# Performance work log

Measured on AMD Instinct MI355X. Metric: run time of the kernel, lower is better.

Reference implementation:

```python
import jax, jax.numpy as jnp
import numpy as np

S, N, DIN, DH, C, K, E = 12, 50000, 64, 128, 2, 3, 600000
HID = (DH + C) // 2  # 65
LN_EPS = 1e-5


def setup_inputs() -> dict:
    key = jax.random.key(0)
    ks = jax.random.split(key, 16)
    sc = 0.05
    inp = {
        'H': jax.random.normal(ks[0], (S, N, DIN), dtype=jnp.float32),
        'edge_index': jax.random.randint(ks[1], (2, E), 0, N, dtype=jnp.int64),
        # stacked gate params, gate order: 0=i, 1=f, 2=c(cell), 3=o
        'Wx': jax.random.normal(ks[2], (4, K, DIN, DH), dtype=jnp.float32) * sc,
        'bx': jnp.zeros((4, DH), dtype=jnp.float32),
        'Wh': jax.random.normal(ks[3], (4, K, DH, DH), dtype=jnp.float32) * sc,
        'bh': jnp.zeros((4, DH), dtype=jnp.float32),
        'b_gate': jnp.zeros((4, DH), dtype=jnp.float32),
        'wc': jax.random.normal(ks[4], (3, DH), dtype=jnp.float32) * sc,  # peephole: i, f, o
        'ln_gamma': jnp.ones((DH,), dtype=jnp.float32),
        'ln_beta': jnp.zeros((DH,), dtype=jnp.float32),
        'W1': jax.random.normal(ks[5], (DH, HID), dtype=jnp.float32) * sc,
        'b1': jnp.zeros((HID,), dtype=jnp.float32),
        'W2': jax.random.normal(ks[6], (HID, C), dtype=jnp.float32) * sc,
        'b2': jnp.zeros((C,), dtype=jnp.float32),
    }
    return inp


def _cheb_norm(edge_index):
    # sym-normalized, lambda_max=2 => scaled Laplacian Lhat = -D^-1/2 A D^-1/2 (zero diagonal)
    src, dst = edge_index[0], edge_index[1]
    ones = jnp.ones((src.shape[0],), dtype=jnp.float32)
    deg = jax.ops.segment_sum(ones, src, num_segments=N)
    dinv = jnp.where(deg > 0, jax.lax.rsqrt(jnp.maximum(deg, 1.0)), 0.0)
    norm = -dinv[src] * dinv[dst]
    return src, dst, norm


def _cheb_conv(x, W, b, src, dst, norm):
    # x: [N, Din]; W: [K, Din, Dout]. T0=x, T1=Lhat x, Tk=2 Lhat T_{k-1} - T_{k-2}
    Tx0 = x
    out = Tx0 @ W[0]
    if K > 1:
        Tx1 = jax.ops.segment_sum(norm[:, None] * Tx0[src], dst, num_segments=N)
        out = out + Tx1 @ W[1]
        for k in range(2, K):
            Tx2 = 2.0 * jax.ops.segment_sum(norm[:, None] * Tx1[src], dst, num_segments=N) - Tx0
            out = out + Tx2 @ W[k]
            Tx0, Tx1 = Tx1, Tx2
    return out + b


def _decoder(H, edge_index, Wx, bx, Wh, bh, b_gate, wc, ln_gamma, ln_beta, W1, b1, W2, b2):
    src, dst, norm = _cheb_norm(edge_index)

    def step(carry, x_t):
        h, c = carry
        gx = lambda g: _cheb_conv(x_t, Wx[g], bx[g], src, dst, norm)
        gh = lambda g: _cheb_conv(h, Wh[g], bh[g], src, dst, norm)
        i = jax.nn.sigmoid(gx(0) + gh(0) + wc[0] * c + b_gate[0])
        f = jax.nn.sigmoid(gx(1) + gh(1) + wc[1] * c + b_gate[1])
        t = jnp.tanh(gx(2) + gh(2) + b_gate[2])
        c = f * c + i * t
        o = jax.nn.sigmoid(gx(3) + gh(3) + wc[2] * c + b_gate[3])
        h = o * jnp.tanh(c)
        return (h, c), h

    h0 = jnp.zeros((N, DH), dtype=H.dtype)
    (_, _), X = jax.lax.scan(step, (h0, h0), H)  # X: [S, N, DH]

    X = jnp.tanh(X)
    # LayerNorm over conv_dim (last axis here)
    mu = jnp.mean(X, axis=-1, keepdims=True)
    var = jnp.mean(jnp.square(X - mu), axis=-1, keepdims=True)
    X = (X - mu) * jax.lax.rsqrt(var + LN_EPS) * ln_gamma + ln_beta
    # dropout in eval mode: identity
    X = jax.nn.relu(X @ W1 + b1) @ W2 + b2  # [S, N, C]
    X = jax.nn.sigmoid(X)
    return jnp.transpose(X, (1, 2, 0))  # [N, C, S]


def reference(H, edge_index, Wx, bx, Wh, bh, b_gate, wc, ln_gamma, ln_beta, W1, b1, W2, b2):
    return _decoder(H, edge_index, Wx, bx, Wh, bh, b_gate, wc, ln_gamma, ln_beta, W1, b1, W2, b2)
```

## Files before the change

### kernel.cpp

```cpp
#include <hip/hip_runtime.h>
#include <cstdint>
#include <cstddef>

#define S_DIM 12
#define N_NODE 50000
#define N_PAD 50048
#define N_P2 50176
#define D_IN 64
#define D_H 128
#define N_E 600000
#define K_TOT 576
#define N_COL 512
#define HID_P 80
#define N_HID 65
#define AXC 192

typedef short bf16x8 __attribute__((ext_vector_type(8)));
typedef float f32x4 __attribute__((ext_vector_type(4)));

__device__ __forceinline__ float bf2f(unsigned short u){
  union { unsigned int i; float f; } v; v.i = ((unsigned int)u) << 16; return v.f;
}
__device__ __forceinline__ unsigned short f2bf(float f){
  union { float f; unsigned int i; } v; v.f = f;
  unsigned int x = v.i;
  return (unsigned short)((x + 0x7fffu + ((x >> 16) & 1u)) >> 16);
}
__device__ __forceinline__ float sigf(float x){ return 1.f/(1.f + __expf(-x)); }
__device__ __forceinline__ float ftanh(float x){
  x = fminf(fmaxf(x, -12.f), 12.f);
  float e = __expf(2.f*x);
  return (e - 1.f)/(e + 1.f);
}

__device__ __forceinline__ void gload16(const void* g, void* lds){
  __builtin_amdgcn_global_load_lds((const __attribute__((address_space(1))) unsigned int*)g,
                                   (__attribute__((address_space(3))) unsigned int*)lds, 16, 0, 0);
}

__device__ __forceinline__ void acc12(float* a, uint2 p0, uint2 p1, uint2 p2, float w){
  unsigned int u[6] = {p0.x, p0.y, p1.x, p1.y, p2.x, p2.y};
#pragma unroll
  for (int i=0;i<6;++i){
    a[2*i]   += w * bf2f((unsigned short)(u[i] & 0xffffu));
    a[2*i+1] += w * bf2f((unsigned short)(u[i] >> 16));
  }
}
__device__ __forceinline__ void acc8(float* a, uint4 h, float w){
  unsigned int u[4] = {h.x, h.y, h.z, h.w};
#pragma unroll
  for (int i=0;i<4;++i){
    a[2*i]   += w * bf2f((unsigned short)(u[i] & 0xffffu));
    a[2*i+1] += w * bf2f((unsigned short)(u[i] >> 16));
  }
}

__global__ void k_prep(const float* __restrict__ Wx, const float* __restrict__ Wh,
                       const float* __restrict__ bx, const float* __restrict__ bh,
                       const float* __restrict__ bg, const float* __restrict__ W1,
                       const float* __restrict__ b1, const float* __restrict__ W2,
                       unsigned short* __restrict__ Bct, float* __restrict__ btot,
                       unsigned short* __restrict__ W1t, float* __restrict__ b1p,
                       float* __restrict__ W2p)
{
  int idx = blockIdx.x*256 + threadIdx.x;
  if (idx < N_COL*K_TOT){
    int cc = idx / K_TOT, k = idx - cc*K_TOT;
    int g = (cc>>4)&3, d = (cc&15) + ((cc>>6)<<4);
    float v;
    if (k < 384){
      int kt = k >> 7, j = k & 127;
      const float* Wg = Wh + (size_t)g*3*128*128;
      if (kt == 0)      v = Wg[(size_t)j*128 + d] - Wg[(size_t)(256+j)*128 + d];
      else if (kt == 1) v = Wg[(size_t)(128+j)*128 + d];
      else              v = 2.f*Wg[(size_t)(256+j)*128 + d];
    } else {
      int kk = k - 384; int kt = kk >> 6, j = kk & 63;
      const float* Wg = Wx + (size_t)g*3*64*128;
      if (kt == 0)      v = Wg[(size_t)j*128 + d] - Wg[(size_t)(128+j)*128 + d];
      else if (kt == 1) v = Wg[(size_t)(64+j)*128 + d];
      else              v = 2.f*Wg[(size_t)(128+j)*128 + d];
    }
    Bct[(size_t)cc*K_TOT + k] = f2bf(v);
  }
  if (idx < N_COL) btot[idx] = bx[idx] + bh[idx] + bg[idx];
  if (idx < HID_P*D_H){ int c = idx >> 7, k = idx & 127;
    W1t[idx] = (c < N_HID) ? f2bf(W1[k*N_HID + c]) : (unsigned short)0; }
  if (idx < HID_P) b1p[idx] = (idx < N_HID) ? b1[idx] : 0.f;
  if (idx < HID_P*2){ int c = idx >> 1, j = idx & 1; W2p[idx] = (c < N_HID) ? W2[c*2 + j] : 0.f; }
}

__global__ void k_xprep(const float* __restrict__ H, unsigned short* __restrict__ Xtr,
                        unsigned short* __restrict__ Axt){
  int idx = blockIdx.x*256 + threadIdx.x;
  if (idx >= N_PAD*64) return;
  int n = idx >> 6, d = idx & 63;
  union { unsigned short u[12]; uint2 q[3]; } pk;
  if (n < N_NODE){
#pragma unroll
    for (int t=0;t<12;++t) pk.u[t] = f2bf(H[((size_t)t*N_NODE + n)*64 + d]);
  } else {
#pragma unroll
    for (int t=0;t<12;++t) pk.u[t] = 0;
  }
  uint2* xp = (uint2*)(Xtr + (size_t)idx*12);
  xp[0]=pk.q[0]; xp[1]=pk.q[1]; xp[2]=pk.q[2];
#pragma unroll
  for (int t=0;t<12;++t) Axt[((size_t)t*N_PAD + n)*AXC + d] = pk.u[t];
  if (n >= N_NODE){
#pragma unroll
    for (int t=0;t<12;++t){
      Axt[((size_t)t*N_PAD + n)*AXC + 64 + d]  = 0;
      Axt[((size_t)t*N_PAD + n)*AXC + 128 + d] = 0;
    }
  }
}

__global__ void k_deg(const int* __restrict__ ei, int* __restrict__ dsrc, int* __restrict__ ddst){
  int e = blockIdx.x*256 + threadIdx.x;
  if (e < N_E){
    atomicAdd(&dsrc[ei[e]], 1);
    atomicAdd(&ddst[ei[N_E + e]], 1);
  }
}
__global__ void k_dinv(const int* __restrict__ dsrc, float* __restrict__ dinv){
  int n = blockIdx.x*256 + threadIdx.x;
  if (n < N_P2) dinv[n] = (dsrc[n] > 0) ? rsqrtf((float)dsrc[n]) : 0.f;
}
__global__ void k_scan1(const int* __restrict__ in, int* __restrict__ outp, int* __restrict__ part){
  __shared__ int sm[256];
  int tid = threadIdx.x;
  int i = blockIdx.x*256 + tid;
  int v = in[i];
  int x = v;
  sm[tid] = x; __syncthreads();
  for (int off=1; off<256; off<<=1){
    int y = (tid >= off) ? sm[tid-off] : 0;
    __syncthreads();
    x += y; sm[tid] = x; __syncthreads();
  }
  outp[i] = x - v;
  if (tid == 255) part[blockIdx.x] = x;
}
__global__ void k_scan2(int* __restrict__ part, int nblk){
  __shared__ int sm[256];
  int tid = threadIdx.x;
  int v = (tid < nblk) ? part[tid] : 0;
// ... 9 lines not shown
  int i = blockIdx.x*256 + threadIdx.x;
  offs[i] = outp[i] + part[blockIdx.x];
}
__global__ void k_csr(const int* __restrict__ ei, const float* __restrict__ dinv,
                      const int* __restrict__ offs, int* __restrict__ cursor,
                      int2* __restrict__ cedge){
  int e = blockIdx.x*256 + threadIdx.x;
  if (e < N_E){
    int s = ei[e], d = ei[N_E + e];
    int pos = atomicAdd(&cursor[d], 1);
    float w = -dinv[s]*dinv[d];
    cedge[offs[d] + pos] = make_int2(s, __float_as_int(w));
  }
}

__global__ void k_xspmm1(const unsigned short* __restrict__ Xtr, unsigned short* __restrict__ Axt,
                         unsigned short* __restrict__ U1tr,
                         const int* __restrict__ offs, const int2* __restrict__ cedge){
  int n = blockIdx.x*4 + (threadIdx.x >> 6);
  int l = threadIdx.x & 63;
  if (n >= N_NODE) return;
  int beg = offs[n], end = offs[n+1];
  int ce = end - 1;
  float a[12];
#pragma unroll
  for (int t=0;t<12;++t) a[t] = 0.f;
  for (int q = beg; q < end; q += 6){
    int2 e0 = cedge[min(q,   ce)];
    int2 e1 = cedge[min(q+1, ce)];
    int2 e2 = cedge[min(q+2, ce)];
    int2 e3 = cedge[min(q+3, ce)];
    int2 e4 = cedge[min(q+4, ce)];
    int2 e5 = cedge[min(q+5, ce)];
    float w0 = __int_as_float(e0.y);
    float w1 = (q+1 < end) ? __int_as_float(e1.y) : 0.f;
    float w2 = (q+2 < end) ? __int_as_float(e2.y) : 0.f;
    float w3 = (q+3 < end) ? __int_as_float(e3.y) : 0.f;
    float w4 = (q+4 < end) ? __int_as_float(e4.y) : 0.f;
    float w5 = (q+5 < end) ? __int_as_float(e5.y) : 0.f;
    const uint2* r0 = (const uint2*)(Xtr + ((size_t)e0.x*64 + l)*12);
    const uint2* r1 = (const uint2*)(Xtr + ((size_t)e1.x*64 + l)*12);
    const uint2* r2 = (const uint2*)(Xtr + ((size_t)e2.x*64 + l)*12);
    const uint2* r3 = (const uint2*)(Xtr + ((size_t)e3.x*64 + l)*12);
    const uint2* r4 = (const uint2*)(Xtr + ((size_t)e4.x*64 + l)*12);
    const uint2* r5 = (const uint2*)(Xtr + ((size_t)e5.x*64 + l)*12);
    uint2 p00=r0[0], p01=r0[1], p02=r0[2];
    uint2 p10=r1[0], p11=r1[1], p12=r1[2];
    uint2 p20=r2[0], p21=r2[1], p22=r2[2];
    uint2 p30=r3[0], p31=r3[1], p32=r3[2];
    uint2 p40=r4[0], p41=r4[1], p42=r4[2];
    uint2 p50=r5[0], p51=r5[1], p52=r5[2];
    acc12(a, p00, p01, p02, w0);
    acc12(a, p10, p11, p12, w1);
    acc12(a, p20, p21, p22, w2);
    acc12(a, p30, p31, p32, w3);
    acc12(a, p40, p41, p42, w4);
    acc12(a, p50, p51, p52, w5);
  }
  union { unsigned short u[12]; uint2 qq[3]; } pk;
#pragma unroll
  for (int t=0;t<12;++t){
    unsigned short b = f2bf(a[t]);
    pk.u[t] = b;
    Axt[((size_t)t*N_PAD + n)*AXC + 64 + l] = b;
  }
  uint2* op = (uint2*)(U1tr + ((size_t)n*64 + l)*12);
  op[0]=pk.qq[0]; op[1]=pk.qq[1]; op[2]=pk.qq[2];
}
__global__ void k_xspmm2(const unsigned short* __restrict__ U1tr, unsigned short* __restrict__ Axt,
                         const int* __restrict__ offs, const int2* __restrict__ cedge){
  int n = blockIdx.x*4 + (threadIdx.x >> 6);
  int l = threadIdx.x & 63;
  if (n >= N_NODE) return;
  int beg = offs[n], end = offs[n+1];
  int ce = end - 1;
  float a[12];
#pragma unroll
  for (int t=0;t<12;++t) a[t] = 0.f;
  for (int q = beg; q < end; q += 6){
    int2 e0 = cedge[min(q,   ce)];
    int2 e1 = cedge[min(q+1, ce)];
    int2 e2 = cedge[min(q+2, ce)];
    int2 e3 = cedge[min(q+3, ce)];
    int2 e4 = cedge[min(q+4, ce)];
    int2 e5 = cedge[min(q+5, ce)];
    float w0 = __int_as_float(e0.y);
    float w1 = (q+1 < end) ? __int_as_float(e1.y) : 0.f;
    float w2 = (q+2 < end) ? __int_as_float(e2.y) : 0.f;
    float w3 = (q+3 < end) ? __int_as_float(e3.y) : 0.f;
    float w4 = (q+4 < end) ? __int_as_float(e4.y) : 0.f;
    float w5 = (q+5 < end) ? __int_as_float(e5.y) : 0.f;
    const uint2* r0 = (const uint2*)(U1tr + ((size_t)e0.x*64 + l)*12);
    const uint2* r1 = (const uint2*)(U1tr + ((size_t)e1.x*64 + l)*12);
    const uint2* r2 = (const uint2*)(U1tr + ((size_t)e2.x*64 + l)*12);
    const uint2* r3 = (const uint2*)(U1tr + ((size_t)e3.x*64 + l)*12);
    const uint2* r4 = (const uint2*)(U1tr + ((size_t)e4.x*64 + l)*12);
    const uint2* r5 = (const uint2*)(U1tr + ((size_t)e5.x*64 + l)*12);
    uint2 p00=r0[0], p01=r0[1], p02=r0[2];
    uint2 p10=r1[0], p11=r1[1], p12=r1[2];
    uint2 p20=r2[0], p21=r2[1], p22=r2[2];
    uint2 p30=r3[0], p31=r3[1], p32=r3[2];
    uint2 p40=r4[0], p41=r4[1], p42=r4[2];
    uint2 p50=r5[0], p51=r5[1], p52=r5[2];
    acc12(a, p00, p01, p02, w0);
    acc12(a, p10, p11, p12, w1);
    acc12(a, p20, p21, p22, w2);
    acc12(a, p30, p31, p32, w3);
    acc12(a, p40, p41, p42, w4);
    acc12(a, p50, p51, p52, w5);
  }
#pragma unroll
  for (int t=0;t<12;++t)
    Axt[((size_t)t*N_PAD + n)*AXC + 128 + l] = f2bf(a[t]);
}

__global__ void k_spmm1(const unsigned short* __restrict__ Hc, unsigned short* __restrict__ U,
                        const int* __restrict__ offs, const int2* __restrict__ cedge){
  int n = blockIdx.x*4 + (threadIdx.x >> 6);
  int l = threadIdx.x & 63;
  if (n >= N_NODE) return;
  int sub = l >> 4, fl = l & 15;
  int beg = offs[n], end = offs[n+1];
  int ce = end - 1;
  float a[8];
#pragma unroll
  for (int j=0;j<8;++j) a[j] = 0.f;
  for (int q = beg; q < end; q += 16){
    int i0 = q + sub, i1 = q + 4 + sub, i2 = q + 8 + sub, i3 = q + 12 + sub;
    int2 e0 = cedge[min(i0, ce)];
    int2 e1 = cedge[min(i1, ce)];
    int2 e2 = cedge[min(i2, ce)];
    int2 e3 = cedge[min(i3, ce)];
    float w0 = (i0 < end) ? __int_as_float(e0.y) : 0.f;
    float w1 = (i1 < end) ? __int_as_float(e1.y) : 0.f;
// ... 8 lines not shown
    acc8(a, h2, w2);
    acc8(a, h3, w3);
  }
#pragma unroll
  for (int j=0;j<8;++j){
    a[j] += __shfl_xor(a[j], 16);
    a[j] += __shfl_xor(a[j], 32);
  }
  if (sub == 0){
    unsigned short o[8];
#pragma unroll
    for (int j=0;j<8;++j) o[j] = f2bf(a[j]);
    *(uint4*)(U + (size_t)n*256 + fl*8) = *(const uint4*)o;
  }
}
__global__ void k_spmm2(unsigned short* __restrict__ U,
                        const int* __restrict__ offs, const int2* __restrict__ cedge){
  int n = blockIdx.x*4 + (threadIdx.x >> 6);
  int l = threadIdx.x & 63;
  if (n >= N_NODE) return;
  int sub = l >> 4, fl = l & 15;
  int beg = offs[n], end = offs[n+1];
  int ce = end - 1;
  float a[8];
#pragma unroll
  for (int j=0;j<8;++j) a[j] = 0.f;
  for (int q = beg; q < end; q += 16){
    int i0 = q + sub, i1 = q + 4 + sub, i2 = q + 8 + sub, i3 = q + 12 + sub;
    int2 e0 = cedge[min(i0, ce)];
    int2 e1 = cedge[min(i1, ce)];
// ... 13 lines not shown
    acc8(a, h3, w3);
  }
#pragma unroll
  for (int j=0;j<8;++j){
    a[j] += __shfl_xor(a[j], 16);
    a[j] += __shfl_xor(a[j], 32);
  }
  if (sub == 0){
    unsigned short o[8];
#pragma unroll
    for (int j=0;j<8;++j) o[j] = f2bf(a[j]);
    *(uint4*)(U + (size_t)n*256 + 128 + fl*8) = *(const uint4*)o;
  }
}

__global__ __launch_bounds__(256,2) void k_gemm(
    const unsigned short* __restrict__ Hc, const unsigned short* __restrict__ U,
    const unsigned short* __restrict__ Axt,
    const unsigned short* __restrict__ Bct, const float* __restrict__ btot,
    const float* __restrict__ wc, float* __restrict__ c, unsigned short* __restrict__ Hn)
{
  __shared__ __align__(16) unsigned short As[2][128*64];
  __shared__ __align__(16) unsigned short Bs[2][128*64];
  int tid = threadIdx.x;
  int w = tid >> 6, l = tid & 63;
  const int NWG = 1564, q8 = NWG >> 3, r8 = NWG & 7;
  int L = blockIdx.y*4 + blockIdx.x;
  int xcd = L & 7, li = L >> 3;
  int W = (xcd < r8 ? xcd*(q8+1) : r8*(q8+1) + (xcd-r8)*q8) + li;
  int bx = W & 3, by = W >> 2;
  int n0 = bx * 128;
  int m0 = by * 128;
  const f32x4 vzero = {0.f,0.f,0.f,0.f};
  f32x4 acc[4][4];
#pragma unroll
  for (int i=0;i<4;++i)
#pragma unroll
    for (int j=0;j<4;++j) acc[i][j] = vzero;
  int wr = w >> 1, wn = w & 1;

  auto stage = [&](int buf, int it){
    const unsigned short* Ab; int astr, acol;
    if (it < 2)      { Ab = Hc;  astr = 128; acol = it*64; }
    else if (it < 6) { Ab = U;   astr = 256; acol = (it-2)*64; }
    else             { Ab = Axt; astr = AXC; acol = (it-6)*64; }
#pragma unroll
    for (int i=0;i<4;++i){
      int rr = w*32 + i*8;
      int row = rr + (l>>3);
      gload16(Ab  + (size_t)(m0+row)*astr + acol + (l&7)*8, (void*)(As[buf] + rr*64));
      gload16(Bct + (size_t)(n0+row)*K_TOT + it*64 + (l&7)*8, (void*)(Bs[buf] + rr*64));
    }
  };

  stage(0, 0);
  __syncthreads();
  for (int it=0; it<9; ++it){
    int cur = it & 1;
    if (it < 8) stage(cur^1, it+1);
#pragma unroll
    for (int kk=0; kk<2; ++kk){
      bf16x8 af[4], bfv[4];
#pragma unroll
      for (int i=0;i<4;++i) af[i]  = *(const bf16x8*)(As[cur] + (wr*64 + i*16 + (l&15))*64 + kk*32 + (l>>4)*8);
#pragma unroll
      for (int j=0;j<4;++j) bfv[j] = *(const bf16x8*)(Bs[cur] + (wn*64 + j*16 + (l&15))*64 + kk*32 + (l>>4)*8);
#pragma unroll
      for (int i=0;i<4;++i)
#pragma unroll
        for (int j=0;j<4;++j)
          acc[i][j] = __builtin_amdgcn_mfma_f32_16x16x32_bf16(af[i], bfv[j], acc[i][j], 0,0,0);
    }
    __syncthreads();
  }
  int dd = (((bx<<1) + wn) << 4) | (l & 15);
  float b_i = btot[dd], b_f = btot[128+dd], b_t = btot[256+dd], b_o = btot[384+dd];
  float wci = wc[dd], wcf = wc[128+dd], wco = wc[256+dd];
#pragma unroll
  for (int i=0;i<4;++i){
    int row0 = m0 + wr*64 + i*16 + (l>>4)*4;
#pragma unroll
    for (int r=0;r<4;++r){
      int row = row0 + r;
      float co = c[(size_t)row*128 + dd];
      float gi = sigf(acc[i][0][r] + b_i + wci*co);
      float gf = sigf(acc[i][1][r] + b_f + wcf*co);
      float tt = ftanh(acc[i][2][r] + b_t);
      float cn = gf*co + gi*tt;
      float go = sigf(acc[i][3][r] + b_o + wco*cn);
      float h = go * ftanh(cn);
      c[(size_t)row*128 + dd] = cn;
      Hn[(size_t)row*128 + dd] = f2bf(h);
    }
  }
}

__global__ __launch_bounds__(256,2) void k_lnmlp(const unsigned short* __restrict__ Hn,
                        const unsigned short* __restrict__ W1t, const float* __restrict__ b1p,
                        const float* __restrict__ W2p, const float* __restrict__ b2,
                        const float* __restrict__ gam, const float* __restrict__ bet,
                        float* __restrict__ out, int t)
{
  __shared__ __align__(16) unsigned short xn[64*128];
  __shared__ __align__(16) unsigned short w1s[HID_P*128];
  __shared__ float w2s[HID_P*2];
  __shared__ float b1s[HID_P];
  __shared__ float b2s[2];
  int tid = threadIdx.x;
  for (int i = tid; i < HID_P*128/8; i += 256) ((int4*)w1s)[i] = ((const int4*)W1t)[i];
  if (tid < HID_P*2) w2s[tid] = W2p[tid];
  if (tid < HID_P)   b1s[tid] = b1p[tid];
  if (tid < 2)       b2s[tid] = b2[tid];
  int n0 = blockIdx.x*64;
  int row = tid >> 2, part = tid & 3;
  int n = n0 + row;
  float vals[32];
  float s = 0.f, ss = 0.f;
  if (n < N_NODE){
    const unsigned short* hp = Hn + (size_t)n*128 + part*32;
#pragma unroll
    for (int k=0;k<32;++k){
      float x = ftanh(bf2f(hp[k]));
      vals[k] = x; s += x; ss += x*x;
    }
  } else {
#pragma unroll
    for (int k=0;k<32;++k) vals[k] = 0.f;
  }
  s  += __shfl_xor(s,1);  s  += __shfl_xor(s,2);
  ss += __shfl_xor(ss,1); ss += __shfl_xor(ss,2);
  float mu = s * (1.f/128.f);
  float var = ss * (1.f/128.f) - mu*mu;
  float inv = rsqrtf(fmaxf(var, 0.f) + 1e-5f);
#pragma unroll
  for (int k=0;k<32;++k){
    int d = part*32 + k;
    xn[row*128 + d] = f2bf((vals[k]-mu)*inv*gam[d] + bet[d]);
  }
  __syncthreads();
  int w = tid >> 6, l = tid & 63;
  const f32x4 vzero = {0.f,0.f,0.f,0.f};
  f32x4 acc[5];
#pragma unroll
  for (int tj=0;tj<5;++tj) acc[tj] = vzero;
#pragma unroll
  for (int kk=0;kk<4;++kk){
    bf16x8 a = *(const bf16x8*)(xn + (w*16 + (l&15))*128 + kk*32 + (l>>4)*8);
#pragma unroll
    for (int tj=0;tj<5;++tj){
      bf16x8 b = *(const bf16x8*)(w1s + (tj*16 + (l&15))*128 + kk*32 + (l>>4)*8);
      acc[tj] = __builtin_amdgcn_mfma_f32_16x16x32_bf16(a, b, acc[tj], 0,0,0);
    }
  }
#pragma unroll
  for (int r=0;r<4;++r){
    int rn = n0 + w*16 + (l>>4)*4 + r;
    float p0 = 0.f, p1 = 0.f;
#pragma unroll
    for (int tj=0;tj<5;++tj){
      int col = tj*16 + (l&15);
      float hv = fmaxf(acc[tj][r] + b1s[col], 0.f);
      p0 += hv * w2s[col*2];
      p1 += hv * w2s[col*2+1];
    }
    p0 += __shfl_xor(p0,1); p0 += __shfl_xor(p0,2); p0 += __shfl_xor(p0,4); p0 += __shfl_xor(p0,8);
    p1 += __shfl_xor(p1,1); p1 += __shfl_xor(p1,2); p1 += __shfl_xor(p1,4); p1 += __shfl_xor(p1,8);
    if ((l & 15) == 0 && rn < N_NODE){
      float* op = out + (size_t)rn*24 + t;
      op[0]  = sigf(p0 + b2s[0]);
      op[12] = sigf(p1 + b2s[1]);
    }
  }
}

extern "C" void kernel_launch(void* const* d_in, const int* in_sizes, int n_in,
                              void* d_out, int out_size, void* d_ws, size_t ws_size,
                              hipStream_t stream)
{
  const float* H   = (const float*)d_in[0];
  const int*   ei  = (const int*)d_in[1];
  const float* Wx  = (const float*)d_in[2];
  const float* bx  = (const float*)d_in[3];
  const float* Wh  = (const float*)d_in[4];
  const float* bh  = (const float*)d_in[5];
  const float* bg  = (const float*)d_in[6];
  const float* wc  = (const float*)d_in[7];
  const float* gam = (const float*)d_in[8];
  const float* bet = (const float*)d_in[9];
  const float* W1  = (const float*)d_in[10];
  const float* b1  = (const float*)d_in[11];
  const float* W2  = (const float*)d_in[12];
  const float* b2  = (const float*)d_in[13];
  float* out = (float*)d_out;
  (void)in_sizes; (void)n_in; (void)out_size; (void)ws_size;

  char* p = (char*)d_ws;
  auto alloc = [&](size_t bytes)->char*{ char* r = p; p += (bytes + 255) & ~(size_t)255; return r; };
  char* zbase = p;
  float*          c_st  = (float*)alloc((size_t)N_PAD*128*4);
  unsigned short* Hbuf0 = (unsigned short*)alloc((size_t)N_PAD*128*2);
  unsigned short* Ubuf  = (unsigned short*)alloc((size_t)N_PAD*256*2);
  int* dsrc   = (int*)alloc((size_t)N_P2*4);
  int* ddst   = (int*)alloc((size_t)N_P2*4);
  int* cursor = (int*)alloc((size_t)N_P2*4);
  size_t zbytes = (size_t)(p - zbase);
  unsigned short* Hbuf1 = (unsigned short*)alloc((size_t)N_PAD*128*2);
  unsigned short* Xtr   = (unsigned short*)alloc((size_t)N_PAD*64*12*2);
  unsigned short* U1tr  = (unsigned short*)alloc((size_t)N_PAD*64*12*2);
  unsigned short* Axt   = (unsigned short*)alloc((size_t)S_DIM*N_PAD*AXC*2);
  unsigned short* Bct   = (unsigned short*)alloc((size_t)N_COL*K_TOT*2);
  float*          btot  = (float*)alloc(N_COL*4);
  unsigned short* W1t   = (unsigned short*)alloc(HID_P*128*2);
  float*          b1p   = (float*)alloc(HID_P*4);
  float*          W2p   = (float*)alloc(HID_P*2*4);
  float*          dinv  = (float*)alloc((size_t)N_P2*4);
  int*            offs  = (int*)alloc((size_t)(N_P2+256)*4);
  int*            outp  = (int*)alloc((size_t)N_P2*4);
  int*            partb = (int*)alloc(256*4);
  int2*           cedge = (int2*)alloc((size_t)N_E*8);

  hipMemsetAsync(zbase, 0, zbytes, stream);
  k_prep<<<(N_COL*K_TOT + 255)/256, 256, 0, stream>>>(Wx, Wh, bx, bh, bg, W1, b1, W2,
                                                      Bct, btot, W1t, b1p, W2p);
  k_xprep<<<(N_PAD*64 + 255)/256, 256, 0, stream>>>(H, Xtr, Axt);
  k_deg<<<(N_E + 255)/256, 256, 0, stream>>>(ei, dsrc, ddst);
  k_dinv<<<N_P2/256, 256, 0, stream>>>(dsrc, dinv);
  k_scan1<<<N_P2/256, 256, 0, stream>>>(ddst, outp, partb);
  k_scan2<<<1, 256, 0, stream>>>(partb, N_P2/256);
  k_scan3<<<N_P2/256, 256, 0, stream>>>(outp, partb, offs);
  k_csr<<<(N_E + 255)/256, 256, 0, stream>>>(ei, dinv, offs, cursor, cedge);
  k_xspmm1<<<N_NODE/4, 256, 0, stream>>>(Xtr, Axt, U1tr, offs, cedge);
  k_xspmm2<<<N_NODE/4, 256, 0, stream>>>(U1tr, Axt, offs, cedge);

  for (int t = 0; t < S_DIM; ++t){
    unsigned short* Hc = (t & 1) ? Hbuf1 : Hbuf0;
    unsigned short* Hn = (t & 1) ? Hbuf0 : Hbuf1;
    if (t > 0){
      k_spmm1<<<N_NODE/4, 256, 0, stream>>>(Hc, Ubuf, offs, cedge);
      k_spmm2<<<N_NODE/4, 256, 0, stream>>>(Ubuf, offs, cedge);
    }
    k_gemm<<<dim3(4, N_PAD/128), 256, 0, stream>>>(Hc, Ubuf,
        Axt + (size_t)t*N_PAD*AXC, Bct, btot, wc, c_st, Hn);
    k_lnmlp<<<N_PAD/64, 256, 0, stream>>>(Hn, W1t, b1p, W2p, b2, gam, bet, out, t);
  }
}
```

Before: 1.976 ms.

## Merge setup kernels, fuse spmm1 with LN-MLP, split x-SpMM halves, single-buffer GEMM

Folds the weight prep, input transpose and degree counting into one multi-role launch, and folds the dinv computation into the first scan pass. The first SpMM of each timestep now runs in the same launch as the LayerNorm+MLP of the previous step. The x-path SpMMs are split into two 6-timestep halves to cut register use. The GEMM drops its LDS double buffering and skips the zero hidden-state part at step 0. The aim is fewer launches and more overlap of independent work. The cost is that loads are no longer overlapped with MFMA inside the GEMM.

Result: faster. 1.860 ms (-5.9%).

```diff
diff --git a/kernel.cpp b/kernel.cpp
--- a/kernel.cpp
+++ b/kernel.cpp
@@ -15,6 +15,12 @@
 #define N_HID 65
 #define AXC 192
 
+#define NB_PREP 1152
+#define NB_XPREP 12512
+#define NB_DEG 2344
+#define NB_SPMM 12500
+#define NB_LN 782
+
 typedef short bf16x8 __attribute__((ext_vector_type(8)));
 typedef float f32x4 __attribute__((ext_vector_type(4)));
 
@@ -32,16 +38,14 @@
   float e = __expf(2.f*x);
   return (e - 1.f)/(e + 1.f);
 }
-
 __device__ __forceinline__ void gload16(const void* g, void* lds){
   __builtin_amdgcn_global_load_lds((const __attribute__((address_space(1))) unsigned int*)g,
                                    (__attribute__((address_space(3))) unsigned int*)lds, 16, 0, 0);
 }
-
-__device__ __forceinline__ void acc12(float* a, uint2 p0, uint2 p1, uint2 p2, float w){
-  unsigned int u[6] = {p0.x, p0.y, p1.x, p1.y, p2.x, p2.y};
-#pragma unroll
-  for (int i=0;i<6;++i){
+__device__ __forceinline__ void acc6(float* a, unsigned int p0, unsigned int p1, unsigned int p2, float w){
+  unsigned int u[3] = {p0, p1, p2};
+#pragma unroll
+  for (int i=0;i<3;++i){
     a[2*i]   += w * bf2f((unsigned short)(u[i] & 0xffffu));
     a[2*i+1] += w * bf2f((unsigned short)(u[i] >> 16));
   }
@@ -55,82 +59,86 @@
   }
 }
 
-__global__ void k_prep(const float* __restrict__ Wx, const float* __restrict__ Wh,
-                       const float* __restrict__ bx, const float* __restrict__ bh,
-                       const float* __restrict__ bg, const float* __restrict__ W1,
-                       const float* __restrict__ b1, const float* __restrict__ W2,
-                       unsigned short* __restrict__ Bct, float* __restrict__ btot,
-                       unsigned short* __restrict__ W1t, float* __restrict__ b1p,
-                       float* __restrict__ W2p)
+__global__ void k_setup(const float* __restrict__ H, const int* __restrict__ ei,
+                        const float* __restrict__ Wx, const float* __restrict__ Wh,
+                        const float* __restrict__ bx, const float* __restrict__ bh,
+                        const float* __restrict__ bg, const float* __restrict__ W1,
+                        const float* __restrict__ b1, const float* __restrict__ W2,
+                        unsigned short* __restrict__ Bct, float* __restrict__ btot,
+                        unsigned short* __restrict__ W1t, float* __restrict__ b1p,
+                        float* __restrict__ W2p, unsigned short* __restrict__ Xtr,
+                        unsigned short* __restrict__ Axt,
+                        int* __restrict__ dsrc, int* __restrict__ ddst)
 {
-  int idx = blockIdx.x*256 + threadIdx.x;
-  if (idx < N_COL*K_TOT){
-    int cc = idx / K_TOT, k = idx - cc*K_TOT;
-    int g = (cc>>4)&3, d = (cc&15) + ((cc>>6)<<4);
-    float v;
-    if (k < 384){
-      int kt = k >> 7, j = k & 127;
-      const float* Wg = Wh + (size_t)g*3*128*128;
-      if (kt == 0)      v = Wg[(size_t)j*128 + d] - Wg[(size_t)(256+j)*128 + d];
-      else if (kt == 1) v = Wg[(size_t)(128+j)*128 + d];
-      else              v = 2.f*Wg[(size_t)(256+j)*128 + d];
+  int bb = blockIdx.x, tid = threadIdx.x;
+  if (bb < NB_PREP){
+    int idx = bb*256 + tid;
+    if (idx < N_COL*K_TOT){
+      int cc = idx / K_TOT, k = idx - cc*K_TOT;
+      int g = (cc>>4)&3, d = (cc&15) + ((cc>>6)<<4);
+      float v;
+      if (k < 384){
+        int kt = k >> 7, j = k & 127;
+        const float* Wg = Wh + (size_t)g*3*128*128;
+        if (kt == 0)      v = Wg[(size_t)j*128 + d] - Wg[(size_t)(256+j)*128 + d];
+        else if (kt == 1) v = Wg[(size_t)(128+j)*128 + d];
+        else              v = 2.f*Wg[(size_t)(256+j)*128 + d];
+      } else {
+        int kk = k - 384; int kt = kk >> 6, j = kk & 63;
+        const float* Wg = Wx + (size_t)g*3*64*128;
+        if (kt == 0)      v = Wg[(size_t)j*128 + d] - Wg[(size_t)(128+j)*128 + d];
+        else if (kt == 1) v = Wg[(size_t)(64+j)*128 + d];
+        else              v = 2.f*Wg[(size_t)(128+j)*128 + d];
+      }
+      Bct[(size_t)cc*K_TOT + k] = f2bf(v);
+    }
+    if (idx < N_COL) btot[idx] = bx[idx] + bh[idx] + bg[idx];
+    if (idx < HID_P*D_H){ int c = idx >> 7, k = idx & 127;
+      W1t[idx] = (c < N_HID) ? f2bf(W1[k*N_HID + c]) : (unsigned short)0; }
+    if (idx < HID_P) b1p[idx] = (idx < N_HID) ? b1[idx] : 0.f;
+    if (idx < HID_P*2){ int c = idx >> 1, j = idx & 1; W2p[idx] = (c < N_HID) ? W2[c*2 + j] : 0.f; }
+  } else if (bb < NB_PREP + NB_XPREP){
+    int idx = (bb - NB_PREP)*256 + tid;
+    int n = idx >> 6, d = idx & 63;
+    unsigned short u[12];
+    if (n < N_NODE){
+#pragma unroll
+      for (int t=0;t<12;++t) u[t] = f2bf(H[((size_t)t*N_NODE + n)*64 + d]);
     } else {
-      int kk = k - 384; int kt = kk >> 6, j = kk & 63;
-      const float* Wg = Wx + (size_t)g*3*64*128;
-      if (kt == 0)      v = Wg[(size_t)j*128 + d] - Wg[(size_t)(128+j)*128 + d];
-      else if (kt == 1) v = Wg[(size_t)(64+j)*128 + d];
-      else              v = 2.f*Wg[(size_t)(128+j)*128 + d];
-    }
-    Bct[(size_t)cc*K_TOT + k] = f2bf(v);
-  }
-  if (idx < N_COL) btot[idx] = bx[idx] + bh[idx] + bg[idx];
-  if (idx < HID_P*D_H){ int c = idx >> 7, k = idx & 127;
-    W1t[idx] = (c < N_HID) ? f2bf(W1[k*N_HID + c]) : (unsigned short)0; }
-  if (idx < HID_P) b1p[idx] = (idx < N_HID) ? b1[idx] : 0.f;
-  if (idx < HID_P*2){ int c = idx >> 1, j = idx & 1; W2p[idx] = (c < N_HID) ? W2[c*2 + j] : 0.f; }
-}
-
-__global__ void k_xprep(const float* __restrict__ H, unsigned short* __restrict__ Xtr,
-                        unsigned short* __restrict__ Axt){
-  int idx = blockIdx.x*256 + threadIdx.x;
-  if (idx >= N_PAD*64) return;
-  int n = idx >> 6, d = idx & 63;
-  union { unsigned short u[12]; uint2 q[3]; } pk;
-  if (n < N_NODE){
-#pragma unroll
-    for (int t=0;t<12;++t) pk.u[t] = f2bf(H[((size_t)t*N_NODE + n)*64 + d]);
+#pragma unroll
+      for (int t=0;t<12;++t) u[t] = 0;
+    }
+    unsigned int* x0 = (unsigned int*)(Xtr + (size_t)idx*6);
+    unsigned int* x1 = (unsigned int*)(Xtr + (size_t)N_PAD*384 + (size_t)idx*6);
+#pragma unroll
+    for (int i=0;i<3;++i){
+      x0[i] = (unsigned int)u[2*i]   | ((unsigned int)u[2*i+1] << 16);
+      x1[i] = (unsigned int)u[6+2*i] | ((unsigned int)u[6+2*i+1] << 16);
+    }
+#pragma unroll
+    for (int t=0;t<12;++t) Axt[((size_t)t*N_PAD + n)*AXC + d] = u[t];
+    if (n >= N_NODE){
+#pragma unroll
+      for (int t=0;t<12;++t){
+        Axt[((size_t)t*N_PAD + n)*AXC + 64 + d]  = 0;
+        Axt[((size_t)t*N_PAD + n)*AXC + 128 + d] = 0;
+      }
+    }
   } else {
-#pragma unroll
-    for (int t=0;t<12;++t) pk.u[t] = 0;
-  }
-  uint2* xp = (uint2*)(Xtr + (size_t)idx*12);
-  xp[0]=pk.q[0]; xp[1]=pk.q[1]; xp[2]=pk.q[2];
-#pragma unroll
-  for (int t=0;t<12;++t) Axt[((size_t)t*N_PAD + n)*AXC + d] = pk.u[t];
-  if (n >= N_NODE){
-#pragma unroll
-    for (int t=0;t<12;++t){
-      Axt[((size_t)t*N_PAD + n)*AXC + 64 + d]  = 0;
-      Axt[((size_t)t*N_PAD + n)*AXC + 128 + d] = 0;
-    }
-  }
-}
-
-__global__ void k_deg(const int* __restrict__ ei, int* __restrict__ dsrc, int* __restrict__ ddst){
-  int e = blockIdx.x*256 + threadIdx.x;
-  if (e < N_E){
-    atomicAdd(&dsrc[ei[e]], 1);
-    atomicAdd(&ddst[ei[N_E + e]], 1);
-  }
-}
-__global__ void k_dinv(const int* __restrict__ dsrc, float* __restrict__ dinv){
-  int n = blockIdx.x*256 + threadIdx.x;
-  if (n < N_P2) dinv[n] = (dsrc[n] > 0) ? rsqrtf((float)dsrc[n]) : 0.f;
-}
-__global__ void k_scan1(const int* __restrict__ in, int* __restrict__ outp, int* __restrict__ part){
+    int e = (bb - NB_PREP - NB_XPREP)*256 + tid;
+    if (e < N_E){
+      atomicAdd(&dsrc[ei[e]], 1);
+      atomicAdd(&ddst[ei[N_E + e]], 1);
+    }
+  }
+}
+
+__global__ void k_scan1d(const int* __restrict__ in, int* __restrict__ outp, int* __restrict__ part,
+                         const int* __restrict__ dsrc, float* __restrict__ dinv){
   __shared__ int sm[256];
   int tid = threadIdx.x;
   int i = blockIdx.x*256 + tid;
+  dinv[i] = (dsrc[i] > 0) ? rsqrtf((float)dsrc[i]) : 0.f;
   int v = in[i];
   int x = v;
   sm[tid] = x; __syncthreads();
@@ -170,17 +178,17 @@
   }
 }
 
-__global__ void k_xspmm1(const unsigned short* __restrict__ Xtr, unsigned short* __restrict__ Axt,
-                         unsigned short* __restrict__ U1tr,
+__global__ void k_xspmm1(const unsigned short* __restrict__ Xh, unsigned short* __restrict__ AxtH,
+                         unsigned short* __restrict__ Uh,
                          const int* __restrict__ offs, const int2* __restrict__ cedge){
   int n = blockIdx.x*4 + (threadIdx.x >> 6);
   int l = threadIdx.x & 63;
   if (n >= N_NODE) return;
   int beg = offs[n], end = offs[n+1];
   int ce = end - 1;
-  float a[12];
-#pragma unroll
-  for (int t=0;t<12;++t) a[t] = 0.f;
+  float a[6];
+#pragma unroll
+  for (int t=0;t<6;++t) a[t] = 0.f;
   for (int q = beg; q < end; q += 6){
     int2 e0 = cedge[min(q,   ce)];
     int2 e1 = cedge[min(q+1, ce)];
@@ -194,45 +202,45 @@
     float w3 = (q+3 < end) ? __int_as_float(e3.y) : 0.f;
     float w4 = (q+4 < end) ? __int_as_float(e4.y) : 0.f;
     float w5 = (q+5 < end) ? __int_as_float(e5.y) : 0.f;
-    const uint2* r0 = (const uint2*)(Xtr + ((size_t)e0.x*64 + l)*12);
-    const uint2* r1 = (const uint2*)(Xtr + ((size_t)e1.x*64 + l)*12);
-    const uint2* r2 = (const uint2*)(Xtr + ((size_t)e2.x*64 + l)*12);
-    const uint2* r3 = (const uint2*)(Xtr + ((size_t)e3.x*64 + l)*12);
-    const uint2* r4 = (const uint2*)(Xtr + ((size_t)e4.x*64 + l)*12);
-    const uint2* r5 = (const uint2*)(Xtr + ((size_t)e5.x*64 + l)*12);
-    uint2 p00=r0[0], p01=r0[1], p02=r0[2];
-    uint2 p10=r1[0], p11=r1[1], p12=r1[2];
-    uint2 p20=r2[0], p21=r2[1], p22=r2[2];
-    uint2 p30=r3[0], p31=r3[1], p32=r3[2];
-    uint2 p40=r4[0], p41=r4[1], p42=r4[2];
-    uint2 p50=r5[0], p51=r5[1], p52=r5[2];
-    acc12(a, p00, p01, p02, w0);
-    acc12(a, p10, p11, p12, w1);
-    acc12(a, p20, p21, p22, w2);
-    acc12(a, p30, p31, p32, w3);
-    acc12(a, p40, p41, p42, w4);
-    acc12(a, p50, p51, p52, w5);
-  }
-  union { unsigned short u[12]; uint2 qq[3]; } pk;
-#pragma unroll
-  for (int t=0;t<12;++t){
-    unsigned short b = f2bf(a[t]);
-    pk.u[t] = b;
-    Axt[((size_t)t*N_PAD + n)*AXC + 64 + l] = b;
-  }
-  uint2* op = (uint2*)(U1tr + ((size_t)n*64 + l)*12);
-  op[0]=pk.qq[0]; op[1]=pk.qq[1]; op[2]=pk.qq[2];
-}
-__global__ void k_xspmm2(const unsigned short* __restrict__ U1tr, unsigned short* __restrict__ Axt,
+    const unsigned int* r0 = (const unsigned int*)(Xh + ((size_t)e0.x*64 + l)*6);
+    const unsigned int* r1 = (const unsigned int*)(Xh + ((size_t)e1.x*64 + l)*6);
+    const unsigned int* r2 = (const unsigned int*)(Xh + ((size_t)e2.x*64 + l)*6);
+    const unsigned int* r3 = (const unsigned int*)(Xh + ((size_t)e3.x*64 + l)*6);
+    const unsigned int* r4 = (const unsigned int*)(Xh + ((size_t)e4.x*64 + l)*6);
+    const unsigned int* r5 = (const unsigned int*)(Xh + ((size_t)e5.x*64 + l)*6);
+    unsigned int p00=r0[0], p01=r0[1], p02=r0[2];
+    unsigned int p10=r1[0], p11=r1[1], p12=r1[2];
+    unsigned int p20=r2[0], p21=r2[1], p22=r2[2];
+    unsigned int p30=r3[0], p31=r3[1], p32=r3[2];
+    unsigned int p40=r4[0], p41=r4[1], p42=r4[2];
+    unsigned int p50=r5[0], p51=r5[1], p52=r5[2];
+    acc6(a, p00, p01, p02, w0);
+    acc6(a, p10, p11, p12, w1);
+    acc6(a, p20, p21, p22, w2);
+    acc6(a, p30, p31, p32, w3);
+    acc6(a, p40, p41, p42, w4);
+    acc6(a, p50, p51, p52, w5);
+  }
+  unsigned short u[6];
+#pragma unroll
+  for (int t=0;t<6;++t){
+    u[t] = f2bf(a[t]);
+    AxtH[((size_t)t*N_PAD + n)*AXC + 64 + l] = u[t];
+  }
+  unsigned int* op = (unsigned int*)(Uh + ((size_t)n*64 + l)*6);
+#pragma unroll
+  for (int i=0;i<3;++i) op[i] = (unsigned int)u[2*i] | ((unsigned int)u[2*i+1] << 16);
+}
+__global__ void k_xspmm2(const unsigned short* __restrict__ Uh, unsigned short* __restrict__ AxtH,
                          const int* __restrict__ offs, const int2* __restrict__ cedge){
   int n = blockIdx.x*4 + (threadIdx.x >> 6);
   int l = threadIdx.x & 63;
   if (n >= N_NODE) return;
   int beg = offs[n], end = offs[n+1];
   int ce = end - 1;
-  float a[12];
-#pragma unroll
-  for (int t=0;t<12;++t) a[t] = 0.f;
+  float a[6];
+#pragma unroll
+  for (int t=0;t<6;++t) a[t] = 0.f;
   for (int q = beg; q < end; q += 6){
     int2 e0 = cedge[min(q,   ce)];
     int2 e1 = cedge[min(q+1, ce)];
@@ -246,34 +254,34 @@
     float w3 = (q+3 < end) ? __int_as_float(e3.y) : 0.f;
     float w4 = (q+4 < end) ? __int_as_float(e4.y) : 0.f;
     float w5 = (q+5 < end) ? __int_as_float(e5.y) : 0.f;
-    const uint2* r0 = (const uint2*)(U1tr + ((size_t)e0.x*64 + l)*12);
-    const uint2* r1 = (const uint2*)(U1tr + ((size_t)e1.x*64 + l)*12);
-    const uint2* r2 = (const uint2*)(U1tr + ((size_t)e2.x*64 + l)*12);
-    const uint2* r3 = (const uint2*)(U1tr + ((size_t)e3.x*64 + l)*12);
-    const uint2* r4 = (const uint2*)(U1tr + ((size_t)e4.x*64 + l)*12);
-    const uint2* r5 = (const uint2*)(U1tr + ((size_t)e5.x*64 + l)*12);
-    uint2 p00=r0[0], p01=r0[1], p02=r0[2];
-    uint2 p10=r1[0], p11=r1[1], p12=r1[2];
-    uint2 p20=r2[0], p21=r2[1], p22=r2[2];
-    uint2 p30=r3[0], p31=r3[1], p32=r3[2];
-    uint2 p40=r4[0], p41=r4[1], p42=r4[2];
-    uint2 p50=r5[0], p51=r5[1], p52=r5[2];
-    acc12(a, p00, p01, p02, w0);
-    acc12(a, p10, p11, p12, w1);
-    acc12(a, p20, p21, p22, w2);
-    acc12(a, p30, p31, p32, w3);
-    acc12(a, p40, p41, p42, w4);
-    acc12(a, p50, p51, p52, w5);
-  }
-#pragma unroll
-  for (int t=0;t<12;++t)
-    Axt[((size_t)t*N_PAD + n)*AXC + 128 + l] = f2bf(a[t]);
-}
-
-__global__ void k_spmm1(const unsigned short* __restrict__ Hc, unsigned short* __restrict__ U,
-                        const int* __restrict__ offs, const int2* __restrict__ cedge){
-  int n = blockIdx.x*4 + (threadIdx.x >> 6);
-  int l = threadIdx.x & 63;
+    const unsigned int* r0 = (const unsigned int*)(Uh + ((size_t)e0.x*64 + l)*6);
+    const unsigned int* r1 = (const unsigned int*)(Uh + ((size_t)e1.x*64 + l)*6);
+    const unsigned int* r2 = (const unsigned int*)(Uh + ((size_t)e2.x*64 + l)*6);
+    const unsigned int* r3 = (const unsigned int*)(Uh + ((size_t)e3.x*64 + l)*6);
+    const unsigned int* r4 = (const unsigned int*)(Uh + ((size_t)e4.x*64 + l)*6);
+    const unsigned int* r5 = (const unsigned int*)(Uh + ((size_t)e5.x*64 + l)*6);
+    unsigned int p00=r0[0], p01=r0[1], p02=r0[2];
+    unsigned int p10=r1[0], p11=r1[1], p12=r1[2];
+    unsigned int p20=r2[0], p21=r2[1], p22=r2[2];
+    unsigned int p30=r3[0], p31=r3[1], p32=r3[2];
+    unsigned int p40=r4[0], p41=r4[1], p42=r4[2];
+    unsigned int p50=r5[0], p51=r5[1], p52=r5[2];
+    acc6(a, p00, p01, p02, w0);
+    acc6(a, p10, p11, p12, w1);
+    acc6(a, p20, p21, p22, w2);
+    acc6(a, p30, p31, p32, w3);
+    acc6(a, p40, p41, p42, w4);
+    acc6(a, p50, p51, p52, w5);
+  }
+#pragma unroll
+  for (int t=0;t<6;++t)
+    AxtH[((size_t)t*N_PAD + n)*AXC + 128 + l] = f2bf(a[t]);
+}
+
+__device__ __forceinline__ void spmm1_body(int n, int l,
+    const unsigned short* __restrict__ Hc, unsigned short* __restrict__ U,
+    const int* __restrict__ offs, const int2* __restrict__ cedge)
+{
   if (n >= N_NODE) return;
   int sub = l >> 4, fl = l & 15;
   int beg = offs[n], end = offs[n+1];
@@ -312,6 +320,7 @@
     *(uint4*)(U + (size_t)n*256 + fl*8) = *(const uint4*)o;
   }
 }
+
 __global__ void k_spmm2(unsigned short* __restrict__ U,
                         const int* __restrict__ offs, const int2* __restrict__ cedge){
   int n = blockIdx.x*4 + (threadIdx.x >> 6);
@@ -355,14 +364,117 @@
   }
 }
 
-__global__ __launch_bounds__(256,2) void k_gemm(
+__device__ __forceinline__ void lnmlp_body(int n0,
+    const unsigned short* __restrict__ Hn,
+    const unsigned short* __restrict__ W1t, const float* __restrict__ b1p,
+    const float* __restrict__ W2p, const float* __restrict__ b2,
+    const float* __restrict__ gam, const float* __restrict__ bet,
+    float* __restrict__ out, int t)
+{
+  __shared__ __align__(16) unsigned short xn[64*128];
+  __shared__ __align__(16) unsigned short w1s[HID_P*128];
+  __shared__ float w2s[HID_P*2];
+  __shared__ float b1s[HID_P];
+  __shared__ float b2s[2];
+  int tid = threadIdx.x;
+  for (int i = tid; i < HID_P*128/8; i += 256) ((int4*)w1s)[i] = ((const int4*)W1t)[i];
+  if (tid < HID_P*2) w2s[tid] = W2p[tid];
+  if (tid < HID_P)   b1s[tid] = b1p[tid];
+  if (tid < 2)       b2s[tid] = b2[tid];
+  int row = tid >> 2, part = tid & 3;
+  int n = n0 + row;
+  float vals[32];
+  float s = 0.f, ss = 0.f;
+  if (n < N_NODE){
+    const unsigned short* hp = Hn + (size_t)n*128 + part*32;
+#pragma unroll
+    for (int k=0;k<32;++k){
+      float x = ftanh(bf2f(hp[k]));
+      vals[k] = x; s += x; ss += x*x;
+    }
+  } else {
+#pragma unroll
+    for (int k=0;k<32;++k) vals[k] = 0.f;
+  }
+  s  += __shfl_xor(s,1);  s  += __shfl_xor(s,2);
+  ss += __shfl_xor(ss,1); ss += __shfl_xor(ss,2);
+  float mu = s * (1.f/128.f);
+  float var = ss * (1.f/128.f) - mu*mu;
+  float inv = rsqrtf(fmaxf(var, 0.f) + 1e-5f);
+#pragma unroll
+  for (int k=0;k<32;++k){
+    int d = part*32 + k;
+    xn[row*128 + d] = f2bf((vals[k]-mu)*inv*gam[d] + bet[d]);
+  }
+  __syncthreads();
+  int w = tid >> 6, l = tid & 63;
+  const f32x4 vzero = {0.f,0.f,0.f,0.f};
+  f32x4 acc[5];
+#pragma unroll
+  for (int tj=0;tj<5;++tj) acc[tj] = vzero;
+#pragma unroll
+  for (int kk=0;kk<4;++kk){
+    bf16x8 a = *(const bf16x8*)(xn + (w*16 + (l&15))*128 + kk*32 + (l>>4)*8);
+#pragma unroll
+    for (int tj=0;tj<5;++tj){
+      bf16x8 b = *(const bf16x8*)(w1s + (tj*16 + (l&15))*128 + kk*32 + (l>>4)*8);
+      acc[tj] = __builtin_amdgcn_mfma_f32_16x16x32_bf16(a, b, acc[tj], 0,0,0);
+    }
+  }
+#pragma unroll
+  for (int r=0;r<4;++r){
+    int rn = n0 + w*16 + (l>>4)*4 + r;
+    float p0 = 0.f, p1 = 0.f;
+#pragma unroll
+    for (int tj=0;tj<5;++tj){
+      int col = tj*16 + (l&15);
+      float hv = fmaxf(acc[tj][r] + b1s[col], 0.f);
+      p0 += hv * w2s[col*2];
+      p1 += hv * w2s[col*2+1];
+    }
+    p0 += __shfl_xor(p0,1); p0 += __shfl_xor(p0,2); p0 += __shfl_xor(p0,4); p0 += __shfl_xor(p0,8);
+    p1 += __shfl_xor(p1,1); p1 += __shfl_xor(p1,2); p1 += __shfl_xor(p1,4); p1 += __shfl_xor(p1,8);
+    if ((l & 15) == 0 && rn < N_NODE){
+      float* op = out + (size_t)rn*24 + t;
+      op[0]  = sigf(p0 + b2s[0]);
+      op[12] = sigf(p1 + b2s[1]);
+    }
+  }
+}
+
+__global__ void k_sp1ln(const unsigned short* __restrict__ Hc, unsigned short* __restrict__ U,
+                        const int* __restrict__ offs, const int2* __restrict__ cedge,
+                        const unsigned short* __restrict__ W1t, const float* __restrict__ b1p,
+                        const float* __restrict__ W2p, const float* __restrict__ b2,
+                        const float* __restrict__ gam, const float* __restrict__ bet,
+                        float* __restrict__ out, int tprev)
+{
+  int bb = blockIdx.x;
+  if (bb < NB_SPMM){
+    spmm1_body(bb*4 + (threadIdx.x >> 6), threadIdx.x & 63, Hc, U, offs, cedge);
+  } else {
+    lnmlp_body((bb - NB_SPMM)*64, Hc, W1t, b1p, W2p, b2, gam, bet, out, tprev);
+  }
+}
+
+__global__ __launch_bounds__(256,2) void k_lnmlp(const unsigned short* __restrict__ Hn,
+                        const unsigned short* __restrict__ W1t, const float* __restrict__ b1p,
+                        const float* __restrict__ W2p, const float* __restrict__ b2,
+                        const float* __restrict__ gam, const float* __restrict__ bet,
+                        float* __restrict__ out, int t)
+{
+  lnmlp_body(blockIdx.x*64, Hn, W1t, b1p, W2p, b2, gam, bet, out, t);
+}
+
+__global__ __launch_bounds__(256,3) void k_gemm(
     const unsigned short* __restrict__ Hc, const unsigned short* __restrict__ U,
     const unsigned short* __restrict__ Axt,
     const unsigned short* __restrict__ Bct, const float* __restrict__ btot,
-    const float* __restrict__ wc, float* __restrict__ c, unsigned short* __restrict__ Hn)
+    const float* __restrict__ wc, float* __restrict__ c, unsigned short* __restrict__ Hn,
+    int it0)
 {
-  __shared__ __align__(16) unsigned short As[2][128*64];
-  __shared__ __align__(16) unsigned short Bs[2][128*64];
+  __shared__ __align__(16) unsigned short As[128*64];
+  __shared__ __align__(16) unsigned short Bs[128*64];
   int tid = threadIdx.x;
   int w = tid >> 6, l = tid & 63;
   const int NWG = 1564, q8 = NWG >> 3, r8 = NWG & 7;
@@ -379,40 +491,33 @@
 #pragma unroll
     for (int j=0;j<4;++j) acc[i][j] = vzero;
   int wr = w >> 1, wn = w & 1;
-
-  auto stage = [&](int buf, int it){
+  for (int it=it0; it<9; ++it){
     const unsigned short* Ab; int astr, acol;
     if (it < 2)      { Ab = Hc;  astr = 128; acol = it*64; }
     else if (it < 6) { Ab = U;   astr = 256; acol = (it-2)*64; }
     else             { Ab = Axt; astr = AXC; acol = (it-6)*64; }
+    if (it != it0) __syncthreads();
 #pragma unroll
     for (int i=0;i<4;++i){
       int rr = w*32 + i*8;
       int row = rr + (l>>3);
-      gload16(Ab  + (size_t)(m0+row)*astr + acol + (l&7)*8, (void*)(As[buf] + rr*64));
-      gload16(Bct + (size_t)(n0+row)*K_TOT + it*64 + (l&7)*8, (void*)(Bs[buf] + rr*64));
-    }
-  };
-
-  stage(0, 0);
-  __syncthreads();
-  for (int it=0; it<9; ++it){
-    int cur = it & 1;
-    if (it < 8) stage(cur^1, it+1);
+      gload16(Ab  + (size_t)(m0+row)*astr + acol + (l&7)*8, (void*)(As + rr*64));
+      gload16(Bct + (size_t)(n0+row)*K_TOT + it*64 + (l&7)*8, (void*)(Bs + rr*64));
+    }
+    __syncthreads();
 #pragma unroll
     for (int kk=0; kk<2; ++kk){
       bf16x8 af[4], bfv[4];
 #pragma unroll
-      for (int i=0;i<4;++i) af[i]  = *(const bf16x8*)(As[cur] + (wr*64 + i*16 + (l&15))*64 + kk*32 + (l>>4)*8);
-#pragma unroll
-      for (int j=0;j<4;++j) bfv[j] = *(const bf16x8*)(Bs[cur] + (wn*64 + j*16 + (l&15))*64 + kk*32 + (l>>4)*8);
+      for (int i=0;i<4;++i) af[i]  = *(const bf16x8*)(As + (wr*64 + i*16 + (l&15))*64 + kk*32 + (l>>4)*8);
+#pragma unroll
+      for (int j=0;j<4;++j) bfv[j] = *(const bf16x8*)(Bs + (wn*64 + j*16 + (l&15))*64 + kk*32 + (l>>4)*8);
 #pragma unroll
       for (int i=0;i<4;++i)
 #pragma unroll
         for (int j=0;j<4;++j)
           acc[i][j] = __builtin_amdgcn_mfma_f32_16x16x32_bf16(af[i], bfv[j], acc[i][j], 0,0,0);
     }
-    __syncthreads();
   }
   int dd = (((bx<<1) + wn) << 4) | (l & 15);
   float b_i = btot[dd], b_f = btot[128+dd], b_t = btot[256+dd], b_o = btot[384+dd];
@@ -432,84 +537,6 @@
       float h = go * ftanh(cn);
       c[(size_t)row*128 + dd] = cn;
       Hn[(size_t)row*128 + dd] = f2bf(h);
-    }
-  }
-}
-
-__global__ __launch_bounds__(256,2) void k_lnmlp(const unsigned short* __restrict__ Hn,
-                        const unsigned short* __restrict__ W1t, const float* __restrict__ b1p,
-                        const float* __restrict__ W2p, const float* __restrict__ b2,
-                        const float* __restrict__ gam, const float* __restrict__ bet,
-                        float* __restrict__ out, int t)
-{
-  __shared__ __align__(16) unsigned short xn[64*128];
-  __shared__ __align__(16) unsigned short w1s[HID_P*128];
-  __shared__ float w2s[HID_P*2];
-  __shared__ float b1s[HID_P];
-  __shared__ float b2s[2];
-  int tid = threadIdx.x;
-  for (int i = tid; i < HID_P*128/8; i += 256) ((int4*)w1s)[i] = ((const int4*)W1t)[i];
-  if (tid < HID_P*2) w2s[tid] = W2p[tid];
-  if (tid < HID_P)   b1s[tid] = b1p[tid];
-  if (tid < 2)       b2s[tid] = b2[tid];
-  int n0 = blockIdx.x*64;
-  int row = tid >> 2, part = tid & 3;
-  int n = n0 + row;
-  float vals[32];
-  float s = 0.f, ss = 0.f;
-  if (n < N_NODE){
-    const unsigned short* hp = Hn + (size_t)n*128 + part*32;
-#pragma unroll
-    for (int k=0;k<32;++k){
-      float x = ftanh(bf2f(hp[k]));
-      vals[k] = x; s += x; ss += x*x;
-    }
-  } else {
-#pragma unroll
-    for (int k=0;k<32;++k) vals[k] = 0.f;
-  }
-  s  += __shfl_xor(s,1);  s  += __shfl_xor(s,2);
-  ss += __shfl_xor(ss,1); ss += __shfl_xor(ss,2);
-  float mu = s * (1.f/128.f);
-  float var = ss * (1.f/128.f) - mu*mu;
-  float inv = rsqrtf(fmaxf(var, 0.f) + 1e-5f);
-#pragma unroll
-  for (int k=0;k<32;++k){
-    int d = part*32 + k;
-    xn[row*128 + d] = f2bf((vals[k]-mu)*inv*gam[d] + bet[d]);
-  }
-  __syncthreads();
-  int w = tid >> 6, l = tid & 63;
-  const f32x4 vzero = {0.f,0.f,0.f,0.f};
-  f32x4 acc[5];
-#pragma unroll
-  for (int tj=0;tj<5;++tj) acc[tj] = vzero;
-#pragma unroll
-  for (int kk=0;kk<4;++kk){
-    bf16x8 a = *(const bf16x8*)(xn + (w*16 + (l&15))*128 + kk*32 + (l>>4)*8);
-#pragma unroll
-    for (int tj=0;tj<5;++tj){
-      bf16x8 b = *(const bf16x8*)(w1s + (tj*16 + (l&15))*128 + kk*32 + (l>>4)*8);
-      acc[tj] = __builtin_amdgcn_mfma_f32_16x16x32_bf16(a, b, acc[tj], 0,0,0);
-    }
-  }
-#pragma unroll
-  for (int r=0;r<4;++r){
-    int rn = n0 + w*16 + (l>>4)*4 + r;
-    float p0 = 0.f, p1 = 0.f;
-#pragma unroll
-    for (int tj=0;tj<5;++tj){
-      int col = tj*16 + (l&15);
-      float hv = fmaxf(acc[tj][r] + b1s[col], 0.f);
-      p0 += hv * w2s[col*2];
-      p1 += hv * w2s[col*2+1];
-    }
-    p0 += __shfl_xor(p0,1); p0 += __shfl_xor(p0,2); p0 += __shfl_xor(p0,4); p0 += __shfl_xor(p0,8);
-    p1 += __shfl_xor(p1,1); p1 += __shfl_xor(p1,2); p1 += __shfl_xor(p1,4); p1 += __shfl_xor(p1,8);
-    if ((l & 15) == 0 && rn < N_NODE){
-      float* op = out + (size_t)rn*24 + t;
-      op[0]  = sigf(p0 + b2s[0]);
-      op[12] = sigf(p1 + b2s[1]);
     }
   }
 }
@@ -538,16 +565,16 @@
   char* p = (char*)d_ws;
   auto alloc = [&](size_t bytes)->char*{ char* r = p; p += (bytes + 255) & ~(size_t)255; return r; };
   char* zbase = p;
-  float*          c_st  = (float*)alloc((size_t)N_PAD*128*4);
-  unsigned short* Hbuf0 = (unsigned short*)alloc((size_t)N_PAD*128*2);
-  unsigned short* Ubuf  = (unsigned short*)alloc((size_t)N_PAD*256*2);
+  float* c_st  = (float*)alloc((size_t)N_PAD*128*4);
   int* dsrc   = (int*)alloc((size_t)N_P2*4);
   int* ddst   = (int*)alloc((size_t)N_P2*4);
   int* cursor = (int*)alloc((size_t)N_P2*4);
   size_t zbytes = (size_t)(p - zbase);
+  unsigned short* Hbuf0 = (unsigned short*)alloc((size_t)N_PAD*128*2);
   unsigned short* Hbuf1 = (unsigned short*)alloc((size_t)N_PAD*128*2);
-  unsigned short* Xtr   = (unsigned short*)alloc((size_t)N_PAD*64*12*2);
-  unsigned short* U1tr  = (unsigned short*)alloc((size_t)N_PAD*64*12*2);
+  unsigned short* Ubuf  = (unsigned short*)alloc((size_t)N_PAD*256*2);
+  unsigned short* Xtr   = (unsigned short*)alloc((size_t)N_PAD*768*2);
+  unsigned short* U1tr  = (unsigned short*)alloc((size_t)N_PAD*768*2);
   unsigned short* Axt   = (unsigned short*)alloc((size_t)S_DIM*N_PAD*AXC*2);
   unsigned short* Bct   = (unsigned short*)alloc((size_t)N_COL*K_TOT*2);
   float*          btot  = (float*)alloc(N_COL*4);
@@ -561,27 +588,31 @@
   int2*           cedge = (int2*)alloc((size_t)N_E*8);
 
   hipMemsetAsync(zbase, 0, zbytes, stream);
-  k_prep<<<(N_COL*K_TOT + 255)/256, 256, 0, stream>>>(Wx, Wh, bx, bh, bg, W1, b1, W2,
-                                                      Bct, btot, W1t, b1p, W2p);
-  k_xprep<<<(N_PAD*64 + 255)/256, 256, 0, stream>>>(H, Xtr, Axt);
-  k_deg<<<(N_E + 255)/256, 256, 0, stream>>>(ei, dsrc, ddst);
-  k_dinv<<<N_P2/256, 256, 0, stream>>>(dsrc, dinv);
-  k_scan1<<<N_P2/256, 256, 0, stream>>>(ddst, outp, partb);
+  k_setup<<<NB_PREP + NB_XPREP + NB_DEG, 256, 0, stream>>>(H, ei, Wx, Wh, bx, bh, bg,
+      W1, b1, W2, Bct, btot, W1t, b1p, W2p, Xtr, Axt, dsrc, ddst);
+  k_scan1d<<<N_P2/256, 256, 0, stream>>>(ddst, outp, partb, dsrc, dinv);
   k_scan2<<<1, 256, 0, stream>>>(partb, N_P2/256);
   k_scan3<<<N_P2/256, 256, 0, stream>>>(outp, partb, offs);
-  k_csr<<<(N_E + 255)/256, 256, 0, stream>>>(ei, dinv, offs, cursor, cedge);
-  k_xspmm1<<<N_NODE/4, 256, 0, stream>>>(Xtr, Axt, U1tr, offs, cedge);
-  k_xspmm2<<<N_NODE/4, 256, 0, stream>>>(U1tr, Axt, offs, cedge);
-
-  for (int t = 0; t < S_DIM; ++t){
+  k_csr<<<NB_DEG, 256, 0, stream>>>(ei, dinv, offs, cursor, cedge);
+  for (int h = 0; h < 2; ++h){
+    k_xspmm1<<<NB_SPMM, 256, 0, stream>>>(Xtr + (size_t)h*N_PAD*384,
+        Axt + (size_t)h*6*N_PAD*AXC, U1tr + (size_t)h*N_PAD*384, offs, cedge);
+  }
+  for (int h = 0; h < 2; ++h){
+    k_xspmm2<<<NB_SPMM, 256, 0, stream>>>(U1tr + (size_t)h*N_PAD*384,
+        Axt + (size_t)h*6*N_PAD*AXC, offs, cedge);
+  }
+
+  k_gemm<<<dim3(4, N_PAD/128), 256, 0, stream>>>(Hbuf0, Ubuf, Axt,
+      Bct, btot, wc, c_st, Hbuf1, 6);
+  for (int t = 1; t < S_DIM; ++t){
     unsigned short* Hc = (t & 1) ? Hbuf1 : Hbuf0;
     unsigned short* Hn = (t & 1) ? Hbuf0 : Hbuf1;
-    if (t > 0){
-      k_spmm1<<<N_NODE/4, 256, 0, stream>>>(Hc, Ubuf, offs, cedge);
-      k_spmm2<<<N_NODE/4, 256, 0, stream>>>(Ubuf, offs, cedge);
-    }
+    k_sp1ln<<<NB_SPMM + NB_LN, 256, 0, stream>>>(Hc, Ubuf, offs, cedge,
+        W1t, b1p, W2p, b2, gam, bet, out, t-1);
+    k_spmm2<<<NB_SPMM, 256, 0, stream>>>(Ubuf, offs, cedge);
     k_gemm<<<dim3(4, N_PAD/128), 256, 0, stream>>>(Hc, Ubuf,
-        Axt + (size_t)t*N_PAD*AXC, Bct, btot, wc, c_st, Hn);
-    k_lnmlp<<<N_PAD/64, 256, 0, stream>>>(Hn, W1t, b1p, W2p, b2, gam, bet, out, t);
-  }
-}
+        Axt + (size_t)t*N_PAD*AXC, Bct, btot, wc, c_st, Hn, 0);
+  }
+  k_lnmlp<<<NB_LN, 256, 0, stream>>>(Hbuf0, W1t, b1p, W2p, b2, gam, bet, out, 11);
+}
```
